# Kernel tuning notes

Measured on AMD Instinct MI355X. Metric: run time of the kernel, lower is better.

## Reference

```python
import jax, jax.numpy as jnp
import numpy as np

N_QUBITS = 5
Q_DEPTH = 1
HALF_PI = np.pi / 2.0

H_GATE = (1.0 / np.sqrt(2.0)) * jnp.array([[1, 1], [1, -1]], dtype=jnp.complex64)
CNOT = jnp.array([[1, 0, 0, 0],
                  [0, 1, 0, 0],
                  [0, 0, 0, 1],
                  [0, 0, 1, 0]], dtype=jnp.complex64).reshape(2, 2, 2, 2)


def _apply_1q(state, gate, wire):
    # state: (2,)*N_QUBITS complex, gate: (2,2) complex
    state = jnp.tensordot(gate, state, axes=([1], [wire]))
    return jnp.moveaxis(state, 0, wire)


def _apply_cnot(state, control, target):
    state = jnp.tensordot(CNOT, state, axes=([2, 3], [control, target]))
    return jnp.moveaxis(state, (0, 1), (control, target))


def _ry(t):
    c = jnp.cos(t / 2).astype(jnp.complex64)
    s = jnp.sin(t / 2).astype(jnp.complex64)
    return jnp.stack([jnp.stack([c, -s]), jnp.stack([s, c])])


def _rx(t):
    c = jnp.cos(t / 2).astype(jnp.complex64)
    js = (-1j) * jnp.sin(t / 2).astype(jnp.complex64)
    return jnp.stack([jnp.stack([c, js]), jnp.stack([js, c])])


def _circuit(angles, q_weights):
    # angles: (N_QUBITS,), q_weights: (Q_DEPTH, N_QUBITS)
    state = jnp.zeros((2,) * N_QUBITS, dtype=jnp.complex64).at[(0,) * N_QUBITS].set(1.0)
    for w in range(N_QUBITS):
        state = _apply_1q(state, H_GATE, w)
    for w in range(N_QUBITS):
        state = _apply_1q(state, _ry(angles[w]), w)
    for k in range(Q_DEPTH):
        # BasicEntanglerLayers: RX rotations then ring of CNOTs
        for w in range(N_QUBITS):
            state = _apply_1q(state, _rx(q_weights[k, w]), w)
        for w in range(N_QUBITS):
            state = _apply_cnot(state, w, (w + 1) % N_QUBITS)
    probs = state.real ** 2 + state.imag ** 2
    zvals = []
    for w in range(N_QUBITS):
        p = probs.sum(axis=tuple(i for i in range(N_QUBITS) if i != w))  # (2,)
        zvals.append(p[0] - p[1])
    return jnp.stack(zvals)  # (N_QUBITS,)


def setup_inputs() -> dict:
    key = jax.random.key(0)
    k1, k2, k3, k4, k5, k6 = jax.random.split(key, 6)
    B = 65536
    return {
        "input_features": jax.random.normal(k1, (B, 512), dtype=jnp.float32),
        "w_pre": jax.random.normal(k2, (N_QUBITS, 512), dtype=jnp.float32) * 0.04,
        "b_pre": jax.random.normal(k3, (N_QUBITS,), dtype=jnp.float32) * 0.04,
        "q_params": 0.01 * jax.random.uniform(k4, (Q_DEPTH * N_QUBITS,), dtype=jnp.float32),
        "w_post": jax.random.normal(k5, (2, N_QUBITS), dtype=jnp.float32) * 0.4,
        "b_post": jax.random.normal(k6, (2,), dtype=jnp.float32) * 0.4,
    }


def reference(input_features, w_pre, b_pre, q_params, w_post, b_post):
    pre_out = input_features @ w_pre.T + b_pre            # (B, 5)
    q_in = jnp.tanh(pre_out) * HALF_PI                    # (B, 5)
    q_weights = q_params.reshape(Q_DEPTH, N_QUBITS)
    q_out = jax.vmap(lambda a: _circuit(a, q_weights))(q_in)  # (B, 5) real
    q_out = q_out.astype(jnp.float32)
    return q_out @ w_post.T + b_post                      # (B, 2)
```

## Files before the change

### kernel.cpp

```cpp
#include <hip/hip_runtime.h>
#include <math.h>

#define NQ 5
#define D 512
#define HALF_PI 1.57079632679489662f

typedef float f32x4 __attribute__((ext_vector_type(4)));


#define DPP_ADD(v, CTRL)                                                        \
    ((v) + __builtin_bit_cast(float, __builtin_amdgcn_update_dpp(               \
               0, __builtin_bit_cast(int, (v)), (CTRL), 0xF, 0xF, true)))

__device__ __forceinline__ float wave_sum(float v) {
    v = DPP_ADD(v, 0xB1);
    v = DPP_ADD(v, 0x4E);
    v = DPP_ADD(v, 0x141);
    v = DPP_ADD(v, 0x140);
    int vi = __builtin_amdgcn_ds_swizzle(__builtin_bit_cast(int, v), 0x401F);
    v = v + __builtin_bit_cast(float, vi);
    const int vb = __builtin_bit_cast(int, v);
    const float lo = __builtin_bit_cast(float, __builtin_amdgcn_readlane(vb, 0));
    const float hi = __builtin_bit_cast(float, __builtin_amdgcn_readlane(vb, 32));
    return lo + hi;
}

__device__ __forceinline__ float uni(float v) {
    return __builtin_bit_cast(float,
        __builtin_amdgcn_readfirstlane(__builtin_bit_cast(int, v)));
}

__device__ __forceinline__ float dot8(f32x4 a, f32x4 b, f32x4 c, f32x4 d) {
    float s;
    s = a.x * b.x;
    s = fmaf(a.y, b.y, s);
    s = fmaf(a.z, b.z, s);
    s = fmaf(a.w, b.w, s);
    s = fmaf(c.x, d.x, s);
    s = fmaf(c.y, d.y, s);
    s = fmaf(c.z, d.z, s);
    s = fmaf(c.w, d.w, s);
    return s;
}

struct Uni {
    float bp[NQ], ct[NQ], wp0[NQ], wp1[NQ], bo0, bo1;
};

__device__ __forceinline__ Uni load_uniforms(const float* b_pre, const float* q_params,
                                             const float* w_post, const float* b_post) {
    Uni u;
#pragma unroll
    for (int q = 0; q < NQ; ++q) {
        u.bp[q]  = uni(b_pre[q]);
        u.ct[q]  = uni(__cosf(q_params[q]));
        u.wp0[q] = uni(w_post[q]);
        u.wp1[q] = uni(w_post[NQ + q]);
    }
    u.bo0 = uni(b_post[0]);
    u.bo1 = uni(b_post[1]);
    return u;
}

__device__ __forceinline__ void compute_pair(
    const f32x4 a0, const f32x4 a1, const f32x4 b0, const f32x4 b1,
    const f32x4 w0[NQ], const f32x4 w1[NQ], const Uni& u,
    float* __restrict__ out, int row0, int lane)
{
    float acc[2][NQ];
#pragma unroll
    for (int q = 0; q < NQ; ++q) {
        acc[0][q] = dot8(a0, w0[q], a1, w1[q]);
        acc[1][q] = dot8(b0, w0[q], b1, w1[q]);
    }
#pragma unroll
    for (int r = 0; r < 2; ++r)
#pragma unroll
        for (int q = 0; q < NQ; ++q)
            acc[r][q] = wave_sum(acc[r][q]);

    float o[2][2];
#pragma unroll
    for (int r = 0; r < 2; ++r) {
        float z[NQ];
#pragma unroll
        for (int q = 0; q < NQ; ++q) {
            const float pv = acc[r][q] + u.bp[q];
            const float e  = __expf(2.0f * pv);
            const float inv = __builtin_amdgcn_rcpf(e + 1.0f);
            const float th = fmaf(-2.0f, inv, 1.0f);
            z[q] = -__sinf(HALF_PI * th) * u.ct[q];
        }
        const float v1   = z[0] * z[1];
        const float z234 = z[2] * z[3] * z[4];
        const float v0   = z[1] * z234;
        const float v2   = v1 * z[2];
        const float v3   = v2 * z[3];
        const float v4   = v1 * z234;

        float s0 = u.bo0, s1 = u.bo1;
        s0 = fmaf(u.wp0[0], v0, s0); s1 = fmaf(u.wp1[0], v0, s1);
        s0 = fmaf(u.wp0[1], v1, s0); s1 = fmaf(u.wp1[1], v1, s1);
        s0 = fmaf(u.wp0[2], v2, s0); s1 = fmaf(u.wp1[2], v2, s1);
        s0 = fmaf(u.wp0[3], v3, s0); s1 = fmaf(u.wp1[3], v3, s1);
        s0 = fmaf(u.wp0[4], v4, s0); s1 = fmaf(u.wp1[4], v4, s1);
        o[r][0] = s0; o[r][1] = s1;
    }

    if (lane == 0) {
        f32x4 dd = { o[0][0], o[0][1], o[1][0], o[1][1] };
        *reinterpret_cast<f32x4*>(out + (size_t)row0 * 2) = dd;
    }
}

template<int ITERS>
__global__ __launch_bounds__(256, 4) void dressed_qnet_fast(
    const float* __restrict__ x, const float* __restrict__ w_pre,
    const float* __restrict__ b_pre, const float* __restrict__ q_params,
    const float* __restrict__ w_post, const float* __restrict__ b_post,
    float* __restrict__ out)
{
    const int lane = threadIdx.x & 63;
    const int wid  = (blockIdx.x * blockDim.x + threadIdx.x) >> 6;
    const int nw   = (gridDim.x * blockDim.x) >> 6;
    const int rstep = 2 * nw;

    const f32x4* xb = reinterpret_cast<const f32x4*>(x);

    f32x4 S[3][4];

#define ISSUE(slot, j)                                                          \
    do {                                                                        \
        const f32x4* p = xb + (size_t)(2 * wid + (j) * rstep) * 128;            \
        S[slot][0] = __builtin_nontemporal_load(p + lane);                      \
        S[slot][1] = __builtin_nontemporal_load(p + lane + 64);                 \
        S[slot][2] = __builtin_nontemporal_load(p + lane + 128);                \
        S[slot][3] = __builtin_nontemporal_load(p + lane + 192);                \
    } while (0)

    ISSUE(0, 0);
    if (ITERS > 1) ISSUE(1, 1);

    f32x4 w0[NQ], w1[NQ];
#pragma unroll
    for (int q = 0; q < NQ; ++q) {
        w0[q] = *reinterpret_cast<const f32x4*>(w_pre + q * D + lane * 4);
        w1[q] = *reinterpret_cast<const f32x4*>(w_pre + q * D + 256 + lane * 4);
    }
    const Uni u = load_uniforms(b_pre, q_params, w_post, b_post);

#pragma unroll
    for (int j = 0; j < ITERS; ++j) {
        const int cs = j % 3;
        const int ns = (j + 2) % 3;
        if (j + 2 < ITERS) ISSUE(ns, j + 2);
        compute_pair(S[cs][0], S[cs][1], S[cs][2], S[cs][3], w0, w1, u,
                     out, 2 * wid + j * rstep, lane);
    }
#undef ISSUE
}

__global__ __launch_bounds__(256, 4) void dressed_qnet_generic(
    const float* __restrict__ x, const float* __restrict__ w_pre,
    const float* __restrict__ b_pre, const float* __restrict__ q_params,
    const float* __restrict__ w_post, const float* __restrict__ b_post,
    float* __restrict__ out, int B)
{
    const int lane = threadIdx.x & 63;
    const int wid  = (blockIdx.x * blockDim.x + threadIdx.x) >> 6;
    const int nw   = (gridDim.x * blockDim.x) >> 6;
    const int rstep = 2 * nw;

    f32x4 w0[NQ], w1[NQ];
#pragma unroll
    for (int q = 0; q < NQ; ++q) {
        w0[q] = *reinterpret_cast<const f32x4*>(w_pre + q * D + lane * 4);
        w1[q] = *reinterpret_cast<const f32x4*>(w_pre + q * D + 256 + lane * 4);
    }
    const Uni u = load_uniforms(b_pre, q_params, w_post, b_post);

    for (int row0 = 2 * wid; row0 < B; row0 += rstep) {
        const f32x4* p = reinterpret_cast<const f32x4*>(x + (size_t)row0 * D);
        const f32x4 a0 = p[lane], a1 = p[lane + 64];
        f32x4 b0, b1;
        const bool have2 = (row0 + 1 < B);
        const int roff = have2 ? 128 : 0;
        b0 = p[lane + roff];
        b1 = p[lane + 64 + roff];

        if (have2) {
            compute_pair(a0, a1, b0, b1, w0, w1, u, out, row0, lane);
        } else {
            float acc[NQ];
#pragma unroll
            for (int q = 0; q < NQ; ++q) acc[q] = wave_sum(dot8(a0, w0[q], a1, w1[q]));
            float z[NQ];
#pragma unroll
            for (int q = 0; q < NQ; ++q) {
                const float pv = acc[q] + u.bp[q];
                const float e  = __expf(2.0f * pv);
                const float inv = __builtin_amdgcn_rcpf(e + 1.0f);
                const float th = fmaf(-2.0f, inv, 1.0f);
                z[q] = -__sinf(HALF_PI * th) * u.ct[q];
            }
            const float v1 = z[0] * z[1];
            const float z234 = z[2] * z[3] * z[4];
            const float v0 = z[1] * z234, v2 = v1 * z[2];
            const float v3 = v2 * z[3],  v4 = v1 * z234;
            float s0 = u.bo0, s1 = u.bo1;
            s0 = fmaf(u.wp0[0], v0, s0); s1 = fmaf(u.wp1[0], v0, s1);
            s0 = fmaf(u.wp0[1], v1, s0); s1 = fmaf(u.wp1[1], v1, s1);
            s0 = fmaf(u.wp0[2], v2, s0); s1 = fmaf(u.wp1[2], v2, s1);
            s0 = fmaf(u.wp0[3], v3, s0); s1 = fmaf(u.wp1[3], v3, s1);
            s0 = fmaf(u.wp0[4], v4, s0); s1 = fmaf(u.wp1[4], v4, s1);
            if (lane == 0) {
                out[(size_t)row0 * 2 + 0] = s0;
                out[(size_t)row0 * 2 + 1] = s1;
            }
        }
    }
}

extern "C" void kernel_launch(void* const* d_in, const int* in_sizes, int n_in,
                              void* d_out, int out_size, void* d_ws, size_t ws_size,
                              hipStream_t stream) {
    const float* x        = (const float*)d_in[0];
    const float* w_pre    = (const float*)d_in[1];
    const float* b_pre    = (const float*)d_in[2];
    const float* q_params = (const float*)d_in[3];
    const float* w_post   = (const float*)d_in[4];
    const float* b_post   = (const float*)d_in[5];
    float* out = (float*)d_out;

    const int B = in_sizes[0] / D;

    const int threads = 256;
    const int blocks  = 512;
    const int nw = blocks * (threads / 64);
    const int rows_per_sweep = 2 * nw;

    if (B == rows_per_sweep * 16) {
        dressed_qnet_fast<16><<<blocks, threads, 0, stream>>>(
            x, w_pre, b_pre, q_params, w_post, b_post, out);
    } else if (B == rows_per_sweep * 8) {
        dressed_qnet_fast<8><<<blocks, threads, 0, stream>>>(
            x, w_pre, b_pre, q_params, w_post, b_post, out);
    } else if (B == rows_per_sweep * 4) {
        dressed_qnet_fast<4><<<blocks, threads, 0, stream>>>(
            x, w_pre, b_pre, q_params, w_post, b_post, out);
    } else if (B == rows_per_sweep * 2) {
        dressed_qnet_fast<2><<<blocks, threads, 0, stream>>>(
            x, w_pre, b_pre, q_params, w_post, b_post, out);
    } else if (B == rows_per_sweep) {
        dressed_qnet_fast<1><<<blocks, threads, 0, stream>>>(
            x, w_pre, b_pre, q_params, w_post, b_post, out);
    } else {
        dressed_qnet_generic<<<2048, threads, 0, stream>>>(
            x, w_pre, b_pre, q_params, w_post, b_post, out, B);
    }
}
```

Baseline: 28.18 us.

## Defer per-row epilogue to distinct lanes and double block count

```diff
diff --git a/kernel.cpp b/kernel.cpp
--- a/kernel.cpp
+++ b/kernel.cpp
@@ -62,55 +62,30 @@
     return u;
 }
 
-__device__ __forceinline__ void compute_pair(
-    const f32x4 a0, const f32x4 a1, const f32x4 b0, const f32x4 b1,
-    const f32x4 w0[NQ], const f32x4 w1[NQ], const Uni& u,
-    float* __restrict__ out, int row0, int lane)
-{
-    float acc[2][NQ];
-#pragma unroll
-    for (int q = 0; q < NQ; ++q) {
-        acc[0][q] = dot8(a0, w0[q], a1, w1[q]);
-        acc[1][q] = dot8(b0, w0[q], b1, w1[q]);
-    }
-#pragma unroll
-    for (int r = 0; r < 2; ++r)
-#pragma unroll
-        for (int q = 0; q < NQ; ++q)
-            acc[r][q] = wave_sum(acc[r][q]);
-
-    float o[2][2];
-#pragma unroll
-    for (int r = 0; r < 2; ++r) {
-        float z[NQ];
-#pragma unroll
-        for (int q = 0; q < NQ; ++q) {
-            const float pv = acc[r][q] + u.bp[q];
-            const float e  = __expf(2.0f * pv);
-            const float inv = __builtin_amdgcn_rcpf(e + 1.0f);
-            const float th = fmaf(-2.0f, inv, 1.0f);
-            z[q] = -__sinf(HALF_PI * th) * u.ct[q];
-        }
-        const float v1   = z[0] * z[1];
-        const float z234 = z[2] * z[3] * z[4];
-        const float v0   = z[1] * z234;
-        const float v2   = v1 * z[2];
-        const float v3   = v2 * z[3];
-        const float v4   = v1 * z234;
-
-        float s0 = u.bo0, s1 = u.bo1;
-        s0 = fmaf(u.wp0[0], v0, s0); s1 = fmaf(u.wp1[0], v0, s1);
-        s0 = fmaf(u.wp0[1], v1, s0); s1 = fmaf(u.wp1[1], v1, s1);
-        s0 = fmaf(u.wp0[2], v2, s0); s1 = fmaf(u.wp1[2], v2, s1);
-        s0 = fmaf(u.wp0[3], v3, s0); s1 = fmaf(u.wp1[3], v3, s1);
-        s0 = fmaf(u.wp0[4], v4, s0); s1 = fmaf(u.wp1[4], v4, s1);
-        o[r][0] = s0; o[r][1] = s1;
-    }
-
-    if (lane == 0) {
-        f32x4 dd = { o[0][0], o[0][1], o[1][0], o[1][1] };
-        *reinterpret_cast<f32x4*>(out + (size_t)row0 * 2) = dd;
-    }
+__device__ __forceinline__ void epilogue(const float dep[NQ], const Uni& u,
+                                         float& o0, float& o1) {
+    float z[NQ];
+#pragma unroll
+    for (int q = 0; q < NQ; ++q) {
+        const float pv = dep[q] + u.bp[q];
+        const float e  = __expf(2.0f * pv);
+        const float inv = __builtin_amdgcn_rcpf(e + 1.0f);
+        const float th = fmaf(-2.0f, inv, 1.0f);
+        z[q] = -__sinf(HALF_PI * th) * u.ct[q];
+    }
+    const float v1   = z[0] * z[1];
+    const float z234 = z[2] * z[3] * z[4];
+    const float v0   = z[1] * z234;
+    const float v2   = v1 * z[2];
+    const float v3   = v2 * z[3];
+    const float v4   = v1 * z234;
+
+    o0 = u.bo0; o1 = u.bo1;
+    o0 = fmaf(u.wp0[0], v0, o0); o1 = fmaf(u.wp1[0], v0, o1);
+    o0 = fmaf(u.wp0[1], v1, o0); o1 = fmaf(u.wp1[1], v1, o1);
+    o0 = fmaf(u.wp0[2], v2, o0); o1 = fmaf(u.wp1[2], v2, o1);
+    o0 = fmaf(u.wp0[3], v3, o0); o1 = fmaf(u.wp1[3], v3, o1);
+    o0 = fmaf(u.wp0[4], v4, o0); o1 = fmaf(u.wp1[4], v4, o1);
 }
 
 template<int ITERS>
@@ -132,10 +107,10 @@
 #define ISSUE(slot, j)                                                          \
     do {                                                                        \
         const f32x4* p = xb + (size_t)(2 * wid + (j) * rstep) * 128;            \
-        S[slot][0] = __builtin_nontemporal_load(p + lane);                      \
-        S[slot][1] = __builtin_nontemporal_load(p + lane + 64);                 \
-        S[slot][2] = __builtin_nontemporal_load(p + lane + 128);                \
-        S[slot][3] = __builtin_nontemporal_load(p + lane + 192);                \
+        S[slot][0] = p[lane];                                                   \
+        S[slot][1] = p[lane + 64];                                              \
+        S[slot][2] = p[lane + 128];                                             \
+        S[slot][3] = p[lane + 192];                                             \
     } while (0)
 
     ISSUE(0, 0);
@@ -148,16 +123,42 @@
         w1[q] = *reinterpret_cast<const f32x4*>(w_pre + q * D + 256 + lane * 4);
     }
     const Uni u = load_uniforms(b_pre, q_params, w_post, b_post);
+
+    float dep[NQ];
+#pragma unroll
+    for (int q = 0; q < NQ; ++q) dep[q] = 0.0f;
 
 #pragma unroll
     for (int j = 0; j < ITERS; ++j) {
         const int cs = j % 3;
         const int ns = (j + 2) % 3;
         if (j + 2 < ITERS) ISSUE(ns, j + 2);
-        compute_pair(S[cs][0], S[cs][1], S[cs][2], S[cs][3], w0, w1, u,
-                     out, 2 * wid + j * rstep, lane);
+
+        float acc[2][NQ];
+#pragma unroll
+        for (int q = 0; q < NQ; ++q) {
+            acc[0][q] = dot8(S[cs][0], w0[q], S[cs][1], w1[q]);
+            acc[1][q] = dot8(S[cs][2], w0[q], S[cs][3], w1[q]);
+        }
+        const bool is0 = (lane == 2 * j);
+        const bool is1 = (lane == 2 * j + 1);
+#pragma unroll
+        for (int q = 0; q < NQ; ++q) {
+            const float r0 = wave_sum(acc[0][q]);
+            const float r1 = wave_sum(acc[1][q]);
+            dep[q] = is0 ? r0 : dep[q];
+            dep[q] = is1 ? r1 : dep[q];
+        }
     }
 #undef ISSUE
+
+    float o0, o1;
+    epilogue(dep, u, o0, o1);
+
+    if (lane < 2 * ITERS) {
+        const int row = 2 * wid + (lane >> 1) * rstep + (lane & 1);
+        *reinterpret_cast<float2*>(out + (size_t)row * 2) = make_float2(o0, o1);
+    }
 }
 
 __global__ __launch_bounds__(256, 4) void dressed_qnet_generic(
@@ -169,7 +170,6 @@
     const int lane = threadIdx.x & 63;
     const int wid  = (blockIdx.x * blockDim.x + threadIdx.x) >> 6;
     const int nw   = (gridDim.x * blockDim.x) >> 6;
-    const int rstep = 2 * nw;
 
     f32x4 w0[NQ], w1[NQ];
 #pragma unroll
@@ -179,45 +179,17 @@
     }
     const Uni u = load_uniforms(b_pre, q_params, w_post, b_post);
 
-    for (int row0 = 2 * wid; row0 < B; row0 += rstep) {
-        const f32x4* p = reinterpret_cast<const f32x4*>(x + (size_t)row0 * D);
+    for (int row = wid; row < B; row += nw) {
+        const f32x4* p = reinterpret_cast<const f32x4*>(x + (size_t)row * D);
         const f32x4 a0 = p[lane], a1 = p[lane + 64];
-        f32x4 b0, b1;
-        const bool have2 = (row0 + 1 < B);
-        const int roff = have2 ? 128 : 0;
-        b0 = p[lane + roff];
-        b1 = p[lane + 64 + roff];
-
-        if (have2) {
-            compute_pair(a0, a1, b0, b1, w0, w1, u, out, row0, lane);
-        } else {
-            float acc[NQ];
-#pragma unroll
-            for (int q = 0; q < NQ; ++q) acc[q] = wave_sum(dot8(a0, w0[q], a1, w1[q]));
-            float z[NQ];
-#pragma unroll
-            for (int q = 0; q < NQ; ++q) {
-                const float pv = acc[q] + u.bp[q];
-                const float e  = __expf(2.0f * pv);
-                const float inv = __builtin_amdgcn_rcpf(e + 1.0f);
-                const float th = fmaf(-2.0f, inv, 1.0f);
-                z[q] = -__sinf(HALF_PI * th) * u.ct[q];
-            }
-            const float v1 = z[0] * z[1];
-            const float z234 = z[2] * z[3] * z[4];
-            const float v0 = z[1] * z234, v2 = v1 * z[2];
-            const float v3 = v2 * z[3],  v4 = v1 * z234;
-            float s0 = u.bo0, s1 = u.bo1;
-            s0 = fmaf(u.wp0[0], v0, s0); s1 = fmaf(u.wp1[0], v0, s1);
-            s0 = fmaf(u.wp0[1], v1, s0); s1 = fmaf(u.wp1[1], v1, s1);
-            s0 = fmaf(u.wp0[2], v2, s0); s1 = fmaf(u.wp1[2], v2, s1);
-            s0 = fmaf(u.wp0[3], v3, s0); s1 = fmaf(u.wp1[3], v3, s1);
-            s0 = fmaf(u.wp0[4], v4, s0); s1 = fmaf(u.wp1[4], v4, s1);
-            if (lane == 0) {
-                out[(size_t)row0 * 2 + 0] = s0;
-                out[(size_t)row0 * 2 + 1] = s1;
-            }
-        }
+        float dep[NQ];
+#pragma unroll
+        for (int q = 0; q < NQ; ++q)
+            dep[q] = wave_sum(dot8(a0, w0[q], a1, w1[q]));
+        float o0, o1;
+        epilogue(dep, u, o0, o1);
+        if (lane == 0)
+            *reinterpret_cast<float2*>(out + (size_t)row * 2) = make_float2(o0, o1);
     }
 }
 
@@ -235,14 +207,11 @@
     const int B = in_sizes[0] / D;
 
     const int threads = 256;
-    const int blocks  = 512;
+    const int blocks  = 1024;
     const int nw = blocks * (threads / 64);
     const int rows_per_sweep = 2 * nw;
 
-    if (B == rows_per_sweep * 16) {
-        dressed_qnet_fast<16><<<blocks, threads, 0, stream>>>(
-            x, w_pre, b_pre, q_params, w_post, b_post, out);
-    } else if (B == rows_per_sweep * 8) {
+    if (B == rows_per_sweep * 8) {
         dressed_qnet_fast<8><<<blocks, threads, 0, stream>>>(
             x, w_pre, b_pre, q_params, w_post, b_post, out);
     } else if (B == rows_per_sweep * 4) {
```

Result: no change. 27.75 us, median of 2 (-1.5%).
